# Performance work log

Hardware: AMD Instinct MI355X
Metric: run time of the kernel (lower is better)

Reference implementation:

```python
import jax, jax.numpy as jnp
import numpy as np

N = 50000   # num_nodes
D = 128     # h_dim
R = 32      # num_rels * 2 (forward + inverse relations)
B = 8       # num_bases
E = 600000  # num_edges


def setup_inputs() -> dict:
    key = jax.random.key(0)
    ks = jax.random.split(key, 14)
    s = 1.0 / np.sqrt(D)
    return {
        "h_ids": jnp.arange(N, dtype=jnp.int32),
        "src": jax.random.randint(ks[0], (E,), 0, N),
        "dst": jax.random.randint(ks[1], (E,), 0, N),
        "etype": jax.random.randint(ks[2], (E,), 0, R),
        "norm": jax.random.uniform(ks[3], (E, 1), dtype=jnp.float32),
        "embedding": jax.random.normal(ks[4], (N, D), dtype=jnp.float32) * 0.05,
        "w_comp1": jax.random.normal(ks[5], (R, B), dtype=jnp.float32) * (1.0 / np.sqrt(B)),
        "bases1": jax.random.normal(ks[6], (B, D, D), dtype=jnp.float32) * s,
        "loop_w1": jax.random.normal(ks[7], (D, D), dtype=jnp.float32) * s,
        "bias1": jnp.zeros((D,), dtype=jnp.float32),
        "w_comp2": jax.random.normal(ks[8], (R, B), dtype=jnp.float32) * (1.0 / np.sqrt(B)),
        "bases2": jax.random.normal(ks[9], (B, D, D), dtype=jnp.float32) * s,
        "loop_w2": jax.random.normal(ks[10], (D, D), dtype=jnp.float32) * s,
        "bias2": jnp.zeros((D,), dtype=jnp.float32),
    }


def _rel_graph_conv(h, src, dst, etype, norm, w_comp, bases, loop_w, bias, act):
    # basis decomposition: W[r] = sum_b w_comp[r,b] * bases[b]
    W = jnp.einsum('rb,bio->rio', w_comp, bases)          # [R, D, D]
    # transform every node by every relation weight (dense GEMM)
    all_t = jnp.einsum('ni,rio->nro', h, W)               # [N, R, D]
    # per-edge gather of relation-specific transformed source features
    msg = all_t[src, etype] * norm                        # [E, D]
    # scatter-aggregate messages at destination nodes
    agg = jax.ops.segment_sum(msg, dst, num_segments=h.shape[0])  # [N, D]
    out = agg + h @ loop_w + bias                         # self-loop + bias
    return act(out) if act is not None else out


def reference(h_ids, src, dst, etype, norm, embedding,
              w_comp1, bases1, loop_w1, bias1,
              w_comp2, bases2, loop_w2, bias2):
    # EmbeddingLayer
    h = embedding[h_ids]                                  # [N, D]
    # hidden layer 0: relu activation (idx < num_hidden_layers-1)
    h = _rel_graph_conv(h, src, dst, etype, norm, w_comp1, bases1, loop_w1, bias1, jax.nn.relu)
    # hidden layer 1: no activation (last layer)
    h = _rel_graph_conv(h, src, dst, etype, norm, w_comp2, bases2, loop_w2, bias2, None)
    return h
```

## Files before the change

kernel.cpp:

```cpp
#include <hip/hip_runtime.h>

#define DD 128
#define NB 8
#define KTOT 1152

typedef unsigned int uint_t;
typedef __attribute__((ext_vector_type(8))) _Float16 half8v;
typedef __attribute__((ext_vector_type(4))) float f32x4;

static __device__ __forceinline__ void gld_lds16(const _Float16* g, _Float16* l)
{
  __builtin_amdgcn_global_load_lds(
      (const __attribute__((address_space(1))) void*)g,
      (__attribute__((address_space(3))) void*)l, 16, 0, 0);
}

__global__ __launch_bounds__(256) void k_prep_w(
    const float* __restrict__ bases1, const float* __restrict__ loopw1,
    const float* __restrict__ bases2, const float* __restrict__ loopw2,
    _Float16* __restrict__ WcA)
{
  int i = blockIdx.x * 256 + threadIdx.x;
  if (i >= 2 * 36 * DD * 32) return;
  int layer = i / (36 * DD * 32);
  int rem   = i % (36 * DD * 32);
  int ks    = rem / (DD * 32);
  int rem2  = rem % (DD * 32);
  int feat  = rem2 / 32;
  int j     = rem2 % 32;
  int k     = ks * 32 + j;
  const float* basesL = layer ? bases2 : bases1;
  const float* loopwL = layer ? loopw2 : loopw1;
  float v;
  if (k < 1024) {
    int kk = k >> 3, b = k & 7;
    v = basesL[((size_t)b * DD + kk) * DD + feat];
  } else {
    v = loopwL[(size_t)(k - 1024) * DD + feat];
  }
  WcA[i] = (_Float16)v;
}

__global__ __launch_bounds__(256) void k_cast(
    const float* __restrict__ h, const int* __restrict__ ids,
    _Float16* __restrict__ hf, int N)
{
  int i = blockIdx.x * 256 + threadIdx.x;
  if (i >= N * (DD / 8)) return;
  int n  = i / (DD / 8);
  int k8 = (i % (DD / 8)) * 8;
  int row = ids ? ids[n] : n;
  const float* hp = h + (size_t)row * DD + k8;
  float4 v0 = *(const float4*)hp;
  float4 v1 = *(const float4*)(hp + 4);
  union { _Float16 e[8]; uint4 q; } p;
  p.e[0]=(_Float16)v0.x; p.e[1]=(_Float16)v0.y; p.e[2]=(_Float16)v0.z; p.e[3]=(_Float16)v0.w;
  p.e[4]=(_Float16)v1.x; p.e[5]=(_Float16)v1.y; p.e[6]=(_Float16)v1.z; p.e[7]=(_Float16)v1.w;
  *(uint4*)&hf[(size_t)n * DD + k8] = p.q;
}

__global__ __launch_bounds__(256) void k_zero(int* __restrict__ p, int n)
{
  int i = blockIdx.x * 256 + threadIdx.x;
  if (i < n) p[i] = 0;
}

__global__ __launch_bounds__(256) void k_hist(
    const int* __restrict__ dst, int* __restrict__ cnt, int E)
{
  int e = blockIdx.x * 256 + threadIdx.x;
  if (e < E) atomicAdd(&cnt[dst[e]], 1);
}

__global__ __launch_bounds__(256) void k_bsum(
    const int* __restrict__ cnt, int* __restrict__ bsum, int N)
{
  __shared__ int s[256];
  int i = blockIdx.x * 256 + threadIdx.x;
  s[threadIdx.x] = (i < N) ? cnt[i] : 0;
  __syncthreads();
  for (int off = 128; off > 0; off >>= 1) {
    if (threadIdx.x < off) s[threadIdx.x] += s[threadIdx.x + off];
    __syncthreads();
  }
  if (threadIdx.x == 0) bsum[blockIdx.x] = s[0];
}

__global__ __launch_bounds__(256) void k_scanb(
    const int* __restrict__ bsum, int* __restrict__ boff, int nb)
{
  __shared__ int s[256];
  int t = threadIdx.x;
  int own = (t < nb) ? bsum[t] : 0;
  s[t] = own;
  __syncthreads();
  for (int off = 1; off < 256; off <<= 1) {
    int v = (t >= off) ? s[t - off] : 0;
    __syncthreads();
    s[t] += v;
    __syncthreads();
  }
  if (t < nb) boff[t] = s[t] - own;
}

__global__ __launch_bounds__(256) void k_scan3(
    const int* __restrict__ cnt, const int* __restrict__ boff,
    int* __restrict__ row_start, int N)
{
  __shared__ int s[256];
  int t = threadIdx.x;
  int i = blockIdx.x * 256 + t;
  int v = (i < N) ? cnt[i] : 0;
  s[t] = v;
  __syncthreads();
  for (int off = 1; off < 256; off <<= 1) {
    int u = (t >= off) ? s[t - off] : 0;
    __syncthreads();
    s[t] += u;
    __syncthreads();
  }
  if (i < N) row_start[i] = boff[blockIdx.x] + s[t] - v;
}

__global__ __launch_bounds__(256) void k_place(
    const int* __restrict__ dst, const int* __restrict__ row_start,
    int* __restrict__ cursor, int* __restrict__ perm, int E)
{
  int e = blockIdx.x * 256 + threadIdx.x;
  if (e < E) {
    int v = dst[e];
    int slot = row_start[v] + atomicAdd(&cursor[v], 1);
    perm[slot] = e;
  }
}

__global__ __launch_bounds__(256) void k_payload(
    const int* __restrict__ perm, const int* __restrict__ src,
    const int* __restrict__ etype, const float* __restrict__ norm,
    const float* __restrict__ wcomp1, const float* __restrict__ wcomp2,
    int* __restrict__ psrc, _Float16* __restrict__ c1, _Float16* __restrict__ c2,
    int E)
{
  int i = blockIdx.x * 256 + threadIdx.x;
  if (i >= E) return;
  int e = perm[i];
  psrc[i] = src[e];
  int t = etype[e];
  float nm = norm[e];
  const float* w1 = wcomp1 + t * NB;
  const float* w2 = wcomp2 + t * NB;
  union { _Float16 h[8]; uint4 q; } p;
  #pragma unroll
  for (int b = 0; b < NB; b++) p.h[b] = (_Float16)(w1[b] * nm);
  *(uint4*)&c1[(size_t)i * 8] = p.q;
  #pragma unroll
  for (int b = 0; b < NB; b++) p.h[b] = (_Float16)(w2[b] * nm);
  *(uint4*)&c2[(size_t)i * 8] = p.q;
}

__global__ __launch_bounds__(256) void k_agg(
    const int* __restrict__ rowst, const int* __restrict__ cnt,
    const int* __restrict__ psrc, const _Float16* __restrict__ c8,
    const _Float16* __restrict__ hf,
    _Float16* __restrict__ agg, int N)
{
  int v = blockIdx.x * 4 + (threadIdx.x >> 6);
  if (v >= N) return;
  int lane = threadIdx.x & 63;
  const uint_t* hf32 = (const uint_t*)hf;
  const int beg = rowst[v];
  const int num = cnt[v];

  float ax[NB] = {}, ay[NB] = {};
  int i = 0;
  for (; i + 4 <= num; i += 4) {
    int s0 = psrc[beg + i],     s1 = psrc[beg + i + 1];
    int s2 = psrc[beg + i + 2], s3 = psrc[beg + i + 3];
    uint_t u0 = hf32[(size_t)s0 * 64 + lane];
    uint_t u1 = hf32[(size_t)s1 * 64 + lane];
    uint_t u2 = hf32[(size_t)s2 * 64 + lane];
    uint_t u3 = hf32[(size_t)s3 * 64 + lane];
    half8v q0 = *(const half8v*)&c8[(size_t)(beg + i) * 8];
    half8v q1 = *(const half8v*)&c8[(size_t)(beg + i + 1) * 8];
    half8v q2 = *(const half8v*)&c8[(size_t)(beg + i + 2) * 8];
    half8v q3 = *(const half8v*)&c8[(size_t)(beg + i + 3) * 8];
    union { uint_t u; _Float16 h[2]; } w;
    w.u = u0; float lo0 = (float)w.h[0], hi0 = (float)w.h[1];
    w.u = u1; float lo1 = (float)w.h[0], hi1 = (float)w.h[1];
    w.u = u2; float lo2 = (float)w.h[0], hi2 = (float)w.h[1];
    w.u = u3; float lo3 = (float)w.h[0], hi3 = (float)w.h[1];
    #pragma unroll
    for (int b = 0; b < NB; b++) {
      float c0 = (float)q0[b], c1_ = (float)q1[b];
      float c2_ = (float)q2[b], c3 = (float)q3[b];
      ax[b] += c0 * lo0 + c1_ * lo1 + c2_ * lo2 + c3 * lo3;
      ay[b] += c0 * hi0 + c1_ * hi1 + c2_ * hi2 + c3 * hi3;
    }
  }
  for (; i < num; i++) {
    int s0 = psrc[beg + i];
    uint_t u0 = hf32[(size_t)s0 * 64 + lane];
    half8v q0 = *(const half8v*)&c8[(size_t)(beg + i) * 8];
    union { uint_t u; _Float16 h[2]; } w;
    w.u = u0; float lo0 = (float)w.h[0], hi0 = (float)w.h[1];
    #pragma unroll
    for (int b = 0; b < NB; b++) {
      float c0 = (float)q0[b];
      ax[b] += c0 * lo0; ay[b] += c0 * hi0;
    }
  }

  union { _Float16 e[8]; uint4 q; } p0, p1;
  #pragma unroll
  for (int b = 0; b < NB; b++) { p0.e[b] = (_Float16)ax[b]; p1.e[b] = (_Float16)ay[b]; }
  uint4* dstp = (uint4*)&agg[(size_t)v * 1024 + lane * 16];
  dstp[0] = p0.q;
  dstp[1] = p1.q;
}

template <int LAYER>
__global__ __launch_bounds__(256) void k_mm(
    const _Float16* __restrict__ agg,
    const _Float16* __restrict__ hf,
    const _Float16* __restrict__ WcA,
    const float* __restrict__ bias,
    float* __restrict__ outf, _Float16* __restrict__ outh, int N)
{
  __shared__ _Float16 sB[2][4096];

  const int n0   = blockIdx.x * 64;
  const int wv   = threadIdx.x >> 6;
  const int lane = threadIdx.x & 63;
  const int l15  = lane & 15, l4 = lane >> 4;

  int nodeL = n0 + lane; if (nodeL >= N) nodeL = N - 1;

  f32x4 acc[2][4];
  #pragma unroll
  for (int a = 0; a < 2; a++)
    #pragma unroll
    for (int b = 0; b < 4; b++) acc[a][b] = (f32x4)0.f;

  const int fbase = wv * 32 + l15;
  const int koff  = l4 * 8;

  auto STAGE = [&](int buf, int t) {
    const _Float16 *g0, *g1;
    if (t < 16) {
      g0 = &agg[(size_t)nodeL * 1024 + (2 * t)     * 32 + wv * 8];
      g1 = &agg[(size_t)nodeL * 1024 + (2 * t + 1) * 32 + wv * 8];
    } else {
      g0 = &hf[(size_t)nodeL * DD + (2 * t - 32) * 32 + wv * 8];
      g1 = &hf[(size_t)nodeL * DD + (2 * t - 31) * 32 + wv * 8];
    }
    gld_lds16(g0, &sB[buf][ wv      * 512]);
    gld_lds16(g1, &sB[buf][(wv + 4) * 512]);
  };

  auto COMPUTE = [&](int buf, int t) {
    #pragma unroll
    for (int sub = 0; sub < 2; sub++) {
      const int ks = 2 * t + sub;
      half8v af[2], bfr[4];
      #pragma unroll
      for (int mf = 0; mf < 2; mf++)
        af[mf] = *(const half8v*)&WcA[((size_t)ks * DD + fbase + mf * 16) * 32 + koff];
      #pragma unroll
      for (int nf = 0; nf < 4; nf++)
        bfr[nf] = *(const half8v*)&sB[buf][(l4 + sub * 4) * 512 + (nf * 16 + l15) * 8];
      #pragma unroll
      for (int mf = 0; mf < 2; mf++)
        #pragma unroll
        for (int nf = 0; nf < 4; nf++)
          acc[mf][nf] = __builtin_amdgcn_mfma_f32_16x16x32_f16(af[mf], bfr[nf], acc[mf][nf], 0, 0, 0);
    }
  };

  STAGE(0, 0);
  __syncthreads();
  int cur = 0;
  for (int t = 0; t < 17; t++) {
    STAGE(cur ^ 1, t + 1);
    COMPUTE(cur, t);
    __syncthreads();
    cur ^= 1;
  }
  COMPUTE(cur, 17);

  #pragma unroll
  for (int mf = 0; mf < 2; mf++)
    #pragma unroll
    for (int nf = 0; nf < 4; nf++) {
      int n = n0 + nf * 16 + l15;
      if (n >= N) continue;
      int feat = wv * 32 + mf * 16 + l4 * 4;
      if (LAYER == 1) {
        union { _Float16 e[4]; uint2 q; } p;
        #pragma unroll
        for (int r = 0; r < 4; r++)
          p.e[r] = (_Float16)fmaxf(acc[mf][nf][r] + bias[feat + r], 0.f);
        *(uint2*)&outh[(size_t)n * DD + feat] = p.q;
      } else {
        float4 o;
        o.x = acc[mf][nf][0] + bias[feat + 0];
        o.y = acc[mf][nf][1] + bias[feat + 1];
        o.z = acc[mf][nf][2] + bias[feat + 2];
        o.w = acc[mf][nf][3] + bias[feat + 3];
        *(float4*)&outf[(size_t)n * DD + feat] = o;
      }
    }
}

extern "C" void kernel_launch(void* const* d_in, const int* in_sizes, int n_in,
                              void* d_out, int out_size, void* d_ws, size_t ws_size,
                              hipStream_t stream)
{
  const int*   h_ids     = (const int*)d_in[0];
  const int*   src       = (const int*)d_in[1];
  const int*   dst       = (const int*)d_in[2];
  const int*   etype     = (const int*)d_in[3];
  const float* norm      = (const float*)d_in[4];
  const float* embedding = (const float*)d_in[5];
  const float* w_comp1   = (const float*)d_in[6];
  const float* bases1    = (const float*)d_in[7];
  const float* loop_w1   = (const float*)d_in[8];
  const float* bias1     = (const float*)d_in[9];
  const float* w_comp2   = (const float*)d_in[10];
  const float* bases2    = (const float*)d_in[11];
  const float* loop_w2   = (const float*)d_in[12];
  const float* bias2     = (const float*)d_in[13];

  const int N = in_sizes[0];
  const int E = in_sizes[1];
  const int NBLK = (N + 255) / 256;

  char* base = (char*)d_ws;
  size_t off = 0;
  auto alloc = [&](size_t bytes) -> char* {
    char* p = base + off;
    off += (bytes + 255) & ~(size_t)255;
    return p;
  };
  _Float16* agg  = (_Float16*)alloc((size_t)N * 1024 * 2);
  _Float16* hfp  = (_Float16*)alloc((size_t)N * DD * 2);
  _Float16* h1h  = (_Float16*)alloc((size_t)N * DD * 2);
  _Float16* WcA  = (_Float16*)alloc((size_t)2 * 36 * DD * 32 * 2);
  int*      cnt    = (int*)   alloc((size_t)2 * N * 4);
  int*      cursor = cnt + N;
  int*      rowst  = (int*)   alloc((size_t)N * 4);
  int*      bsum   = (int*)   alloc(256 * 4);
  int*      boff   = (int*)   alloc(256 * 4);
  int*      perm   = (int*)   alloc((size_t)E * 4);
  int*      psrc   = (int*)   alloc((size_t)E * 4);
  _Float16* c1     = (_Float16*)alloc((size_t)E * 8 * 2);
  _Float16* c2     = (_Float16*)alloc((size_t)E * 8 * 2);
  float*    out    = (float*)d_out;

  k_zero <<<(2 * N + 255) / 256, 256, 0, stream>>>(cnt, 2 * N);
  k_hist <<<(E + 255) / 256, 256, 0, stream>>>(dst, cnt, E);
  k_bsum <<<NBLK, 256, 0, stream>>>(cnt, bsum, N);
  k_scanb<<<1, 256, 0, stream>>>(bsum, boff, NBLK);
  k_scan3<<<NBLK, 256, 0, stream>>>(cnt, boff, rowst, N);
  k_place<<<(E + 255) / 256, 256, 0, stream>>>(dst, rowst, cursor, perm, E);
  k_payload<<<(E + 255) / 256, 256, 0, stream>>>(perm, src, etype, norm,
                                                 w_comp1, w_comp2, psrc, c1, c2, E);

  k_prep_w<<<(2 * 36 * DD * 32 + 255) / 256, 256, 0, stream>>>(bases1, loop_w1, bases2, loop_w2, WcA);

  dim3 gmm((N + 63) / 64);
  int gagg = (N + 3) / 4;

  k_cast<<<(N * (DD / 8) + 255) / 256, 256, 0, stream>>>(embedding, h_ids, hfp, N);
  k_agg<<<gagg, 256, 0, stream>>>(rowst, cnt, psrc, c1, hfp, agg, N);
  k_mm<1><<<gmm, 256, 0, stream>>>(agg, hfp, WcA, bias1, nullptr, h1h, N);

  k_agg<<<gagg, 256, 0, stream>>>(rowst, cnt, psrc, c2, h1h, agg, N);
  k_mm<2><<<gmm, 256, 0, stream>>>(agg, h1h, WcA + (size_t)36 * DD * 32, bias2, out, nullptr, N);
}
```

Baseline: 287.6 us.

## Pair edges per destination and use packed fp16 dot2 in aggregation

Pads each destination's edge list to an even count and stores per-edge basis coefficients interleaved in pairs, so the aggregation kernel can combine two edges per v_dot2 instruction after byte-permuting their gathered features. It also fuses the placement and payload kernels, which removes the perm array and one indirect read. The padding needs extra zero-fill kernels over the enlarged psrc and coefficient buffers. Payload stores become scattered 2-byte writes, and the fp16 dot-product accumulation changes numerics slightly.

Measured after the change: 290.6 us. No clear change (+1.0%).

```diff
diff --git a/kernel.cpp b/kernel.cpp
--- a/kernel.cpp
+++ b/kernel.cpp
@@ -6,6 +6,7 @@
 
 typedef unsigned int uint_t;
 typedef __attribute__((ext_vector_type(8))) _Float16 half8v;
+typedef __attribute__((ext_vector_type(2))) _Float16 half2v;
 typedef __attribute__((ext_vector_type(4))) float f32x4;
 
 static __device__ __forceinline__ void gld_lds16(const _Float16* g, _Float16* l)
@@ -13,6 +14,21 @@
   __builtin_amdgcn_global_load_lds(
       (const __attribute__((address_space(1))) void*)g,
       (__attribute__((address_space(3))) void*)l, 16, 0, 0);
+}
+
+static __device__ __forceinline__ half2v bc_h2(uint_t u)
+{
+  union { uint_t u; half2v h; } c; c.u = u; return c.h;
+}
+
+static __device__ __forceinline__ float fdot2(uint_t a, uint_t b, float acc)
+{
+#if __has_builtin(__builtin_amdgcn_fdot2)
+  return __builtin_amdgcn_fdot2(bc_h2(a), bc_h2(b), acc, false);
+#else
+  half2v x = bc_h2(a), y = bc_h2(b);
+  return acc + (float)x[0] * (float)y[0] + (float)x[1] * (float)y[1];
+#endif
 }
 
 __global__ __launch_bounds__(256) void k_prep_w(
@@ -77,7 +93,7 @@
 {
   __shared__ int s[256];
   int i = blockIdx.x * 256 + threadIdx.x;
-  s[threadIdx.x] = (i < N) ? cnt[i] : 0;
+  s[threadIdx.x] = (i < N) ? ((cnt[i] + 1) & ~1) : 0;
   __syncthreads();
   for (int off = 128; off > 0; off >>= 1) {
     if (threadIdx.x < off) s[threadIdx.x] += s[threadIdx.x + off];
@@ -110,7 +126,7 @@
   __shared__ int s[256];
   int t = threadIdx.x;
   int i = blockIdx.x * 256 + t;
-  int v = (i < N) ? cnt[i] : 0;
+  int v = (i < N) ? ((cnt[i] + 1) & ~1) : 0;
   s[t] = v;
   __syncthreads();
   for (int off = 1; off < 256; off <<= 1) {
@@ -122,45 +138,33 @@
   if (i < N) row_start[i] = boff[blockIdx.x] + s[t] - v;
 }
 
-__global__ __launch_bounds__(256) void k_place(
-    const int* __restrict__ dst, const int* __restrict__ row_start,
-    int* __restrict__ cursor, int* __restrict__ perm, int E)
-{
-  int e = blockIdx.x * 256 + threadIdx.x;
-  if (e < E) {
-    int v = dst[e];
-    int slot = row_start[v] + atomicAdd(&cursor[v], 1);
-    perm[slot] = e;
-  }
-}
-
-__global__ __launch_bounds__(256) void k_payload(
-    const int* __restrict__ perm, const int* __restrict__ src,
+__global__ __launch_bounds__(256) void k_place_payload(
+    const int* __restrict__ dst, const int* __restrict__ src,
     const int* __restrict__ etype, const float* __restrict__ norm,
     const float* __restrict__ wcomp1, const float* __restrict__ wcomp2,
+    const int* __restrict__ rowst, int* __restrict__ cursor,
     int* __restrict__ psrc, _Float16* __restrict__ c1, _Float16* __restrict__ c2,
     int E)
 {
-  int i = blockIdx.x * 256 + threadIdx.x;
-  if (i >= E) return;
-  int e = perm[i];
-  psrc[i] = src[e];
+  int e = blockIdx.x * 256 + threadIdx.x;
+  if (e >= E) return;
+  int v = dst[e];
+  int slot = rowst[v] + atomicAdd(&cursor[v], 1);
+  psrc[slot] = src[e];
   int t = etype[e];
   float nm = norm[e];
   const float* w1 = wcomp1 + t * NB;
   const float* w2 = wcomp2 + t * NB;
-  union { _Float16 h[8]; uint4 q; } p;
-  #pragma unroll
-  for (int b = 0; b < NB; b++) p.h[b] = (_Float16)(w1[b] * nm);
-  *(uint4*)&c1[(size_t)i * 8] = p.q;
-  #pragma unroll
-  for (int b = 0; b < NB; b++) p.h[b] = (_Float16)(w2[b] * nm);
-  *(uint4*)&c2[(size_t)i * 8] = p.q;
+  size_t base = (size_t)(slot >> 1) * 16 + (slot & 1);
+  #pragma unroll
+  for (int b = 0; b < NB; b++) c1[base + b * 2] = (_Float16)(w1[b] * nm);
+  #pragma unroll
+  for (int b = 0; b < NB; b++) c2[base + b * 2] = (_Float16)(w2[b] * nm);
 }
 
 __global__ __launch_bounds__(256) void k_agg(
     const int* __restrict__ rowst, const int* __restrict__ cnt,
-    const int* __restrict__ psrc, const _Float16* __restrict__ c8,
+    const int* __restrict__ psrc, const _Float16* __restrict__ cpair,
     const _Float16* __restrict__ hf,
     _Float16* __restrict__ agg, int N)
 {
@@ -169,44 +173,44 @@
   int lane = threadIdx.x & 63;
   const uint_t* hf32 = (const uint_t*)hf;
   const int beg = rowst[v];
-  const int num = cnt[v];
+  const int npairs = (cnt[v] + 1) >> 1;
+  const uint_t* cp = (const uint_t*)cpair + (size_t)(beg >> 1) * 8;
+  const int* ps = psrc + beg;
 
   float ax[NB] = {}, ay[NB] = {};
   int i = 0;
-  for (; i + 4 <= num; i += 4) {
-    int s0 = psrc[beg + i],     s1 = psrc[beg + i + 1];
-    int s2 = psrc[beg + i + 2], s3 = psrc[beg + i + 3];
+  for (; i + 2 <= npairs; i += 2) {
+    int s0 = ps[2*i + 0], s1 = ps[2*i + 1];
+    int s2 = ps[2*i + 2], s3 = ps[2*i + 3];
     uint_t u0 = hf32[(size_t)s0 * 64 + lane];
     uint_t u1 = hf32[(size_t)s1 * 64 + lane];
     uint_t u2 = hf32[(size_t)s2 * 64 + lane];
     uint_t u3 = hf32[(size_t)s3 * 64 + lane];
-    half8v q0 = *(const half8v*)&c8[(size_t)(beg + i) * 8];
-    half8v q1 = *(const half8v*)&c8[(size_t)(beg + i + 1) * 8];
-    half8v q2 = *(const half8v*)&c8[(size_t)(beg + i + 2) * 8];
-    half8v q3 = *(const half8v*)&c8[(size_t)(beg + i + 3) * 8];
-    union { uint_t u; _Float16 h[2]; } w;
-    w.u = u0; float lo0 = (float)w.h[0], hi0 = (float)w.h[1];
-    w.u = u1; float lo1 = (float)w.h[0], hi1 = (float)w.h[1];
-    w.u = u2; float lo2 = (float)w.h[0], hi2 = (float)w.h[1];
-    w.u = u3; float lo3 = (float)w.h[0], hi3 = (float)w.h[1];
+    uint_t lo01 = __builtin_amdgcn_perm(u0, u1, 0x01000504);
+    uint_t hi01 = __builtin_amdgcn_perm(u0, u1, 0x03020706);
+    uint_t lo23 = __builtin_amdgcn_perm(u2, u3, 0x01000504);
+    uint_t hi23 = __builtin_amdgcn_perm(u2, u3, 0x03020706);
     #pragma unroll
     for (int b = 0; b < NB; b++) {
-      float c0 = (float)q0[b], c1_ = (float)q1[b];
-      float c2_ = (float)q2[b], c3 = (float)q3[b];
-      ax[b] += c0 * lo0 + c1_ * lo1 + c2_ * lo2 + c3 * lo3;
-      ay[b] += c0 * hi0 + c1_ * hi1 + c2_ * hi2 + c3 * hi3;
-    }
-  }
-  for (; i < num; i++) {
-    int s0 = psrc[beg + i];
+      uint_t ca = cp[(size_t)i * 8 + b];
+      uint_t cb = cp[(size_t)(i + 1) * 8 + b];
+      ax[b] = fdot2(ca, lo01, ax[b]);
+      ay[b] = fdot2(ca, hi01, ay[b]);
+      ax[b] = fdot2(cb, lo23, ax[b]);
+      ay[b] = fdot2(cb, hi23, ay[b]);
+    }
+  }
+  if (i < npairs) {
+    int s0 = ps[2*i + 0], s1 = ps[2*i + 1];
     uint_t u0 = hf32[(size_t)s0 * 64 + lane];
-    half8v q0 = *(const half8v*)&c8[(size_t)(beg + i) * 8];
-    union { uint_t u; _Float16 h[2]; } w;
-    w.u = u0; float lo0 = (float)w.h[0], hi0 = (float)w.h[1];
+    uint_t u1 = hf32[(size_t)s1 * 64 + lane];
+    uint_t lo01 = __builtin_amdgcn_perm(u0, u1, 0x01000504);
+    uint_t hi01 = __builtin_amdgcn_perm(u0, u1, 0x03020706);
     #pragma unroll
     for (int b = 0; b < NB; b++) {
-      float c0 = (float)q0[b];
-      ax[b] += c0 * lo0; ay[b] += c0 * hi0;
+      uint_t ca = cp[(size_t)i * 8 + b];
+      ax[b] = fdot2(ca, lo01, ax[b]);
+      ay[b] = fdot2(ca, hi01, ay[b]);
     }
   }
 
@@ -332,6 +336,7 @@
 
   const int N = in_sizes[0];
   const int E = in_sizes[1];
+  const int S = E + N;
   const int NBLK = (N + 255) / 256;
 
   char* base = (char*)d_ws;
@@ -350,20 +355,21 @@
   int*      rowst  = (int*)   alloc((size_t)N * 4);
   int*      bsum   = (int*)   alloc(256 * 4);
   int*      boff   = (int*)   alloc(256 * 4);
-  int*      perm   = (int*)   alloc((size_t)E * 4);
-  int*      psrc   = (int*)   alloc((size_t)E * 4);
-  _Float16* c1     = (_Float16*)alloc((size_t)E * 8 * 2);
-  _Float16* c2     = (_Float16*)alloc((size_t)E * 8 * 2);
+  int*      psrc   = (int*)   alloc((size_t)S * 4);
+  _Float16* c1     = (_Float16*)alloc((size_t)S * 8 * 2);
+  _Float16* c2     = (_Float16*)alloc((size_t)S * 8 * 2);
   float*    out    = (float*)d_out;
 
   k_zero <<<(2 * N + 255) / 256, 256, 0, stream>>>(cnt, 2 * N);
+  k_zero <<<(S + 255) / 256, 256, 0, stream>>>(psrc, S);
+  k_zero <<<(S * 4 + 255) / 256, 256, 0, stream>>>((int*)c1, S * 4);
+  k_zero <<<(S * 4 + 255) / 256, 256, 0, stream>>>((int*)c2, S * 4);
   k_hist <<<(E + 255) / 256, 256, 0, stream>>>(dst, cnt, E);
   k_bsum <<<NBLK, 256, 0, stream>>>(cnt, bsum, N);
   k_scanb<<<1, 256, 0, stream>>>(bsum, boff, NBLK);
   k_scan3<<<NBLK, 256, 0, stream>>>(cnt, boff, rowst, N);
-  k_place<<<(E + 255) / 256, 256, 0, stream>>>(dst, rowst, cursor, perm, E);
-  k_payload<<<(E + 255) / 256, 256, 0, stream>>>(perm, src, etype, norm,
-                                                 w_comp1, w_comp2, psrc, c1, c2, E);
+  k_place_payload<<<(E + 255) / 256, 256, 0, stream>>>(
+      dst, src, etype, norm, w_comp1, w_comp2, rowst, cursor, psrc, c1, c2, E);
 
   k_prep_w<<<(2 * 36 * DD * 32 + 255) / 256, 256, 0, stream>>>(bases1, loop_w1, bases2, loop_w2, WcA);
 
```
